# Optimization experiments

Measured on AMD Instinct MI355X. Metric: run time of the kernel, lower is better.

Reference implementation:

```python
import jax, jax.numpy as jnp
import numpy as np

B, N, K, H, NC, NL = 512, 128, 16, 16, 6, 4  # batch, atoms, neighbors/atom, h_a, classes, EGNN layers

def _lin(key, fi, fo):
    lim = 1.0 / np.sqrt(fi)
    return jax.random.uniform(key, (fi, fo), jnp.float32, -lim, lim)

def _bias(key, fi, fo):
    lim = 1.0 / np.sqrt(fi)
    return jax.random.uniform(key, (fo,), jnp.float32, -lim, lim)

def setup_inputs():
    key = jax.random.key(0)
    kc, ke, ki, ko, kf, kl = jax.random.split(key, 6)
    coords = jax.random.normal(kc, (B, N, 3), dtype=jnp.float32)
    # fixed adjacency: node i -> (i+1 .. i+K) mod N, same for every frame
    adj = np.zeros((N, N), dtype=np.float32)
    idx = np.arange(N)
    for d in range(1, K + 1):
        adj[idx, (idx + d) % N] = 1.0
    data = jnp.concatenate([coords, jnp.broadcast_to(jnp.asarray(adj), (B, N, N))], axis=-1)  # [B,N,3+N]
    # edge-index construction (host-side; matches torch (edge_inds>0).nonzero().t(), row/col += offset*N)
    off, r, c = np.nonzero(np.broadcast_to(adj > 0.0, (B, N, N)))
    row = jnp.asarray(r + off * N, dtype=jnp.int32)
    col = jnp.asarray(c + off * N, dtype=jnp.int32)
    emb_w = jax.random.normal(ke, (N, H), dtype=jnp.float32)  # atom_emb.weight.data.normal_()
    k1, k2 = jax.random.split(ki); ein_w, ein_b = _lin(k1, H, H), _bias(k2, H, H)
    k1, k2 = jax.random.split(ko); eout_w, eout_b = _lin(k1, H, H), _bias(k2, H, H)
    k1, k2 = jax.random.split(kf); fc_w, fc_b = _lin(k1, H, NC), _bias(k2, H, NC)
    def make_layer(k):
        ks = jax.random.split(k, 11)
        xav = 0.001 * np.sqrt(6.0 / (H + 1))  # coord_mlp last layer: xavier_uniform gain=0.001, no bias
        return dict(
            e1_w=_lin(ks[0], 2 * H + 2, H), e1_b=_bias(ks[1], 2 * H + 2, H),
            e2_w=_lin(ks[2], H, H),        e2_b=_bias(ks[3], H, H),
            n1_w=_lin(ks[4], 2 * H, H),    n1_b=_bias(ks[5], 2 * H, H),
            n2_w=_lin(ks[6], H, H),        n2_b=_bias(ks[7], H, H),
            c1_w=_lin(ks[8], H, H),        c1_b=_bias(ks[9], H, H),
            c2_w=jax.random.uniform(ks[10], (H, 1), jnp.float32, -xav, xav))
    layers = [make_layer(k) for k in jax.random.split(kl, NL)]
    stacked = {name: jnp.stack([l[name] for l in layers]) for name in layers[0]}  # [NL, ...]
    out = dict(data=data, row=row, col=col, emb_w=emb_w, ein_w=ein_w, ein_b=ein_b,
               eout_w=eout_w, eout_b=eout_b, fc_w=fc_w, fc_b=fc_b)
    out.update(stacked)
    return out

def reference(data, row, col, emb_w, ein_w, ein_b, eout_w, eout_b, fc_w, fc_b,
              e1_w, e1_b, e2_w, e2_b, n1_w, n1_b, n2_w, n2_b, c1_w, c1_b, c2_w):
    Bn = data.shape[0] * data.shape[1]  # B*N flattened nodes
    silu = jax.nn.silu
    seg = lambda v: jax.ops.segment_sum(v, row, num_segments=Bn)
    # atom_emb(arange(N)) repeated over batch -> tile embedding table rows
    h = jnp.broadcast_to(emb_w[None, :, :], (data.shape[0], data.shape[1], H)).reshape(Bn, H)
    x = data[:, :, :3].reshape(Bn, 3).astype(jnp.float32)
    e_attr = jnp.ones((row.shape[0], 1), jnp.float32)
    cnt = jnp.maximum(seg(jnp.ones((row.shape[0],), jnp.float32)), 1.0)[:, None]  # for coords_agg='mean'
    h = h @ ein_w + ein_b  # embedding_in
    for l in range(NL):  # E_GCL layers (residual=True, attention=False)
        cd = x[row] - x[col]                                  # [E,3] coord_diff
        radial = jnp.sum(cd * cd, axis=1, keepdims=True)      # [E,1]
        ein = jnp.concatenate([h[row], h[col], radial, e_attr], axis=1)  # [E, 2H+2]
        m = silu(silu(ein @ e1_w[l] + e1_b[l]) @ e2_w[l] + e2_b[l])      # edge_mlp -> [E,H]
        t = silu(m @ c1_w[l] + c1_b[l]) @ c2_w[l]             # coord_mlp -> [E,1]
        x = x + seg(cd * t) / cnt                             # mean-aggregated coord update
        agg_m = seg(m)                                        # scatter-add messages to nodes
        h = h + (silu(jnp.concatenate([h, agg_m], axis=1) @ n1_w[l] + n1_b[l]) @ n2_w[l] + n2_b[l])
    h = h @ eout_w + eout_b  # embedding_out
    prot = jnp.sum(h.reshape(data.shape[0], data.shape[1], H), axis=1) / N  # pooling
    return jax.nn.softmax(prot @ fc_w + fc_b, axis=-1)
```

## Files before the change

kernel.cpp:

```cpp
#include <hip/hip_runtime.h>
#include <math.h>


#define NB   512
#define NT   512
#define NN   128
#define HH   16
#define NCLS 6
#define NLAY 4
#define PAD  20

#define W_E1   0
#define W_E1B  544
#define W_E2   560
#define W_E2B  816
#define W_C1   832
#define W_C1B  1088
#define W_C2   1104
#define W_N1   1120
#define W_N1B  1632
#define W_N2   1648
#define W_N2B  1904
#define W_TOT  1920

__device__ __forceinline__ float silu_f(float v) {
    return __fdividef(v, 1.f + __expf(-v));
}

extern "C" __global__ __launch_bounds__(512, 4)
void GraphVampNet_73624329388105_kernel(
    const float* __restrict__ data,
    const float* __restrict__ emb_w,
    const float* __restrict__ ein_w, const float* __restrict__ ein_b,
    const float* __restrict__ eout_w, const float* __restrict__ eout_b,
    const float* __restrict__ fc_w,  const float* __restrict__ fc_b,
    const float* __restrict__ e1_w,  const float* __restrict__ e1_b,
    const float* __restrict__ e2_w,  const float* __restrict__ e2_b,
    const float* __restrict__ n1_w,  const float* __restrict__ n1_b,
    const float* __restrict__ n2_w,  const float* __restrict__ n2_b,
    const float* __restrict__ c1_w,  const float* __restrict__ c1_b,
    const float* __restrict__ c2_w,
    float* __restrict__ out)
{
    __shared__ float h[NN][PAD];
    __shared__ float xs[NN][4];
    __shared__ float pB[NN][PAD];
    __shared__ __align__(16) float un[384 * PAD];
    __shared__ __align__(16) float wb[W_TOT];
    __shared__ float hp[HH];
    __shared__ float prot[HH];

    const int b = blockIdx.x;
    const int t = threadIdx.x;

    if (t < NN) {
        const float* dp = data + ((size_t)b * NN + t) * (NN + 3);
        xs[t][0] = dp[0]; xs[t][1] = dp[1]; xs[t][2] = dp[2]; xs[t][3] = 0.f;

        float ev[HH];
        #pragma unroll
        for (int k = 0; k < HH; k++) ev[k] = emb_w[t * HH + k];
        float acc[HH];
        #pragma unroll
        for (int o = 0; o < HH; o++) acc[o] = ein_b[o];
        #pragma unroll
        for (int k = 0; k < HH; k++) {
            const float v = ev[k];
            #pragma unroll
            for (int o = 0; o < HH; o++) acc[o] += v * ein_w[k * HH + o];
        }
        #pragma unroll
        for (int o = 0; o < HH; o++) h[t][o] = acc[o];
    }

    const int i = t & (NN - 1);
    const int q = t >> 7;

    for (int l = 0; l < NLAY; l++) {
        {
            const float* E1W = e1_w + l * 34 * HH;
            wb[W_E1 + t] = E1W[t];
            if (t < 32) wb[W_E1 + 512 + t] = E1W[512 + t];
            wb[W_N1 + t] = n1_w[l * 2 * HH * HH + t];
            if (t < 256) {
                wb[W_E2 + t] = e2_w[l * HH * HH + t];
                wb[W_C1 + t] = c1_w[l * HH * HH + t];
                wb[W_N2 + t] = n2_w[l * HH * HH + t];
            }
            if (t < HH) {
                wb[W_E1B + t] = e1_b[l * HH + t];
                wb[W_E2B + t] = e2_b[l * HH + t];
                wb[W_C1B + t] = c1_b[l * HH + t];
                wb[W_C2  + t] = c2_w[l * HH + t];
                wb[W_N1B + t] = n1_b[l * HH + t];
                wb[W_N2B + t] = n2_b[l * HH + t];
            }
        }
        __syncthreads();

        if (t < 2 * NN) {
            const int node = t & (NN - 1);
            float hv[HH];
            #pragma unroll
            for (int k = 0; k < HH; k++) hv[k] = h[node][k];
            if (t < NN) {
                float acc[HH];
                #pragma unroll
                for (int o = 0; o < HH; o++) acc[o] = wb[W_E1B + o] + wb[W_E1 + 33 * HH + o];
                #pragma unroll
                for (int k = 0; k < HH; k++) {
                    const float v = hv[k];
                    #pragma unroll
                    for (int o = 0; o < HH; o++) acc[o] += v * wb[W_E1 + k * HH + o];
                }
                #pragma unroll
                for (int o = 0; o < HH; o++) un[node * PAD + o] = acc[o];
            } else {
                float acc[HH];
                #pragma unroll
                for (int o = 0; o < HH; o++) acc[o] = 0.f;
                #pragma unroll
                for (int k = 0; k < HH; k++) {
                    const float v = hv[k];
                    #pragma unroll
                    for (int o = 0; o < HH; o++) acc[o] += v * wb[W_E1 + (16 + k) * HH + o];
                }
                #pragma unroll
                for (int o = 0; o < HH; o++) pB[node][o] = acc[o];
            }
        }
        __syncthreads();

        float aggm[HH];
        #pragma unroll
        for (int o = 0; o < HH; o++) aggm[o] = 0.f;
        float cx0 = 0.f, cx1 = 0.f, cx2 = 0.f;
        {
            const float4 xi = *(const float4*)&xs[i][0];

            #pragma unroll 1
            for (int g = 0; g < 2; g++) {
                unsigned o_col = W_E1 + 32 * HH;
                unsigned o_e2  = W_E2,  o_e2b = W_E2B;
                unsigned o_c1  = W_C1,  o_c1b = W_C1B;
                unsigned o_c2  = W_C2;
                unsigned o_pa  = (unsigned)(i * PAD);
                asm volatile("" : "+v"(o_col), "+v"(o_e2), "+v"(o_e2b),
                                  "+v"(o_c1), "+v"(o_c1b), "+v"(o_c2), "+v"(o_pa));

                const int dbase = q * 4 + g * 2 + 1;
                const int j0 = (i + dbase) & (NN - 1);
                const int j1 = (i + dbase + 1) & (NN - 1);
                const float4 xj0 = *(const float4*)&xs[j0][0];
                const float4 xj1 = *(const float4*)&xs[j1][0];
                const float a00 = xi.x - xj0.x, a01 = xi.y - xj0.y, a02 = xi.z - xj0.z;
                const float a10 = xi.x - xj1.x, a11 = xi.y - xj1.y, a12 = xi.z - xj1.z;
                const float r0 = a00 * a00 + a01 * a01 + a02 * a02;
                const float r1 = a10 * a10 + a11 * a11 + a12 * a12;

                float m0[HH], m1v[HH];
                #pragma unroll
                for (int qq = 0; qq < 4; qq++) {
                    const float4 pa = ((const float4*)(un + o_pa))[qq];
                    const float4 wc = ((const float4*)(wb + o_col))[qq];
                    const float4 p0 = *(const float4*)&pB[j0][qq * 4];
                    const float4 p1 = *(const float4*)&pB[j1][qq * 4];
                    m0[qq*4+0]  = silu_f(pa.x + p0.x + r0 * wc.x);
                    m0[qq*4+1]  = silu_f(pa.y + p0.y + r0 * wc.y);
                    m0[qq*4+2]  = silu_f(pa.z + p0.z + r0 * wc.z);
                    m0[qq*4+3]  = silu_f(pa.w + p0.w + r0 * wc.w);
                    m1v[qq*4+0] = silu_f(pa.x + p1.x + r1 * wc.x);
                    m1v[qq*4+1] = silu_f(pa.y + p1.y + r1 * wc.y);
                    m1v[qq*4+2] = silu_f(pa.z + p1.z + r1 * wc.z);
                    m1v[qq*4+3] = silu_f(pa.w + p1.w + r1 * wc.w);
                }

                float ac0[HH], ac1[HH];
                #pragma unroll
                for (int qq = 0; qq < 4; qq++) {
                    const float4 bb = ((const float4*)(wb + o_e2b))[qq];
                    ac0[qq*4+0] = bb.x; ac0[qq*4+1] = bb.y; ac0[qq*4+2] = bb.z; ac0[qq*4+3] = bb.w;
                    ac1[qq*4+0] = bb.x; ac1[qq*4+1] = bb.y; ac1[qq*4+2] = bb.z; ac1[qq*4+3] = bb.w;
                }
                #pragma unroll
                for (int k = 0; k < HH; k++) {
                    const float v0 = m0[k], v1 = m1v[k];
                    #pragma unroll
                    for (int qq = 0; qq < 4; qq++) {
                        const float4 w = ((const float4*)(wb + o_e2))[k * 4 + qq];
                        ac0[qq*4+0] += v0 * w.x; ac0[qq*4+1] += v0 * w.y;
                        ac0[qq*4+2] += v0 * w.z; ac0[qq*4+3] += v0 * w.w;
                        ac1[qq*4+0] += v1 * w.x; ac1[qq*4+1] += v1 * w.y;
                        ac1[qq*4+2] += v1 * w.z; ac1[qq*4+3] += v1 * w.w;
                    }
                }
                #pragma unroll
                for (int o = 0; o < HH; o++) {
                    m0[o]  = silu_f(ac0[o]);
                    m1v[o] = silu_f(ac1[o]);
                    aggm[o] += m0[o] + m1v[o];
                }

                #pragma unroll
                for (int qq = 0; qq < 4; qq++) {
                    const float4 bb = ((const float4*)(wb + o_c1b))[qq];
                    ac0[qq*4+0] = bb.x; ac0[qq*4+1] = bb.y; ac0[qq*4+2] = bb.z; ac0[qq*4+3] = bb.w;
                    ac1[qq*4+0] = bb.x; ac1[qq*4+1] = bb.y; ac1[qq*4+2] = bb.z; ac1[qq*4+3] = bb.w;
                }
                #pragma unroll
                for (int k = 0; k < HH; k++) {
                    const float v0 = m0[k], v1 = m1v[k];
                    #pragma unroll
                    for (int qq = 0; qq < 4; qq++) {
                        const float4 w = ((const float4*)(wb + o_c1))[k * 4 + qq];
                        ac0[qq*4+0] += v0 * w.x; ac0[qq*4+1] += v0 * w.y;
                        ac0[qq*4+2] += v0 * w.z; ac0[qq*4+3] += v0 * w.w;
                        ac1[qq*4+0] += v1 * w.x; ac1[qq*4+1] += v1 * w.y;
                        ac1[qq*4+2] += v1 * w.z; ac1[qq*4+3] += v1 * w.w;
                    }
                }
                float t0 = 0.f, t1 = 0.f;
                #pragma unroll
                for (int qq = 0; qq < 4; qq++) {
                    const float4 cw = ((const float4*)(wb + o_c2))[qq];
                    t0 += silu_f(ac0[qq*4+0]) * cw.x + silu_f(ac0[qq*4+1]) * cw.y
                        + silu_f(ac0[qq*4+2]) * cw.z + silu_f(ac0[qq*4+3]) * cw.w;
                    t1 += silu_f(ac1[qq*4+0]) * cw.x + silu_f(ac1[qq*4+1]) * cw.y
                        + silu_f(ac1[qq*4+2]) * cw.z + silu_f(ac1[qq*4+3]) * cw.w;
                }

                cx0 += a00 * t0 + a10 * t1;
                cx1 += a01 * t0 + a11 * t1;
                cx2 += a02 * t0 + a12 * t1;
            }
        }
        __syncthreads();

        if (t >= NN) {
            const int r = t - NN;
            #pragma unroll
            for (int o = 0; o < HH; o++) un[r * PAD + o] = aggm[o];
            float4 cxv; cxv.x = cx0; cxv.y = cx1; cxv.z = cx2; cxv.w = 0.f;
            *(float4*)(un + r * PAD + 16) = cxv;
        }
        __syncthreads();

        if (t < NN) {
            float aggt[HH];
            #pragma unroll
            for (int o = 0; o < HH; o++)
                aggt[o] = aggm[o] + un[t * PAD + o] + un[(t + 128) * PAD + o]
                        + un[(t + 256) * PAD + o];
            const float sx0 = cx0 + un[t * PAD + 16] + un[(t + 128) * PAD + 16]
                            + un[(t + 256) * PAD + 16];
            const float sx1 = cx1 + un[t * PAD + 17] + un[(t + 128) * PAD + 17]
                            + un[(t + 256) * PAD + 17];
            const float sx2 = cx2 + un[t * PAD + 18] + un[(t + 128) * PAD + 18]
                            + un[(t + 256) * PAD + 18];

            float hv[HH];
            #pragma unroll
            for (int k = 0; k < HH; k++) hv[k] = h[t][k];

            float acc[HH];
            #pragma unroll
            for (int o = 0; o < HH; o++) acc[o] = wb[W_N1B + o];
            #pragma unroll
            for (int k = 0; k < HH; k++) {
                const float v = hv[k];
                #pragma unroll
                for (int o = 0; o < HH; o++) acc[o] += v * wb[W_N1 + k * HH + o];
            }
            #pragma unroll
            for (int k = 0; k < HH; k++) {
                const float v = aggt[k];
                #pragma unroll
                for (int o = 0; o < HH; o++) acc[o] += v * wb[W_N1 + (16 + k) * HH + o];
            }
            float u[HH];
            #pragma unroll
            for (int o = 0; o < HH; o++) u[o] = silu_f(acc[o]);

            float acc2[HH];
            #pragma unroll
            for (int o = 0; o < HH; o++) acc2[o] = wb[W_N2B + o];
            #pragma unroll
            for (int k = 0; k < HH; k++) {
                const float v = u[k];
                #pragma unroll
                for (int o = 0; o < HH; o++) acc2[o] += v * wb[W_N2 + k * HH + o];
            }
            #pragma unroll
            for (int o = 0; o < HH; o++) h[t][o] = hv[o] + acc2[o];

            const float inv = 1.f / 16.f;
            xs[t][0] += sx0 * inv;
            xs[t][1] += sx1 * inv;
            xs[t][2] += sx2 * inv;
        }
        __syncthreads();
    }

    if (t < HH) {
        float acc = 0.f;
        for (int n = 0; n < NN; n++) acc += h[n][t];
        hp[t] = acc * (1.f / NN);
    }
    __syncthreads();
    if (t < HH) {
        float acc = eout_b[t];
        #pragma unroll
        for (int k = 0; k < HH; k++) acc += hp[k] * eout_w[k * HH + t];
        prot[t] = acc;
    }
    __syncthreads();
    if (t == 0) {
        float lg[NCLS];
        float mx = -1e30f;
        #pragma unroll
        for (int c = 0; c < NCLS; c++) {
            float acc = fc_b[c];
            #pragma unroll
            for (int k = 0; k < HH; k++) acc += prot[k] * fc_w[k * NCLS + c];
            lg[c] = acc;
            mx = fmaxf(mx, acc);
        }
        float s = 0.f;
        #pragma unroll
        for (int c = 0; c < NCLS; c++) { lg[c] = __expf(lg[c] - mx); s += lg[c]; }
        const float invs = 1.f / s;
        #pragma unroll
        for (int c = 0; c < NCLS; c++) out[b * NCLS + c] = lg[c] * invs;
    }
}

extern "C" void kernel_launch(void* const* d_in, const int* in_sizes, int n_in,
                              void* d_out, int out_size, void* d_ws, size_t ws_size,
                              hipStream_t stream) {
    const float* data   = (const float*)d_in[0];
    const float* emb_w  = (const float*)d_in[3];
    const float* ein_w  = (const float*)d_in[4];
    const float* ein_b  = (const float*)d_in[5];
    const float* eout_w = (const float*)d_in[6];
    const float* eout_b = (const float*)d_in[7];
    const float* fc_w   = (const float*)d_in[8];
    const float* fc_b   = (const float*)d_in[9];
    const float* e1_w   = (const float*)d_in[10];
    const float* e1_b   = (const float*)d_in[11];
    const float* e2_w   = (const float*)d_in[12];
    const float* e2_b   = (const float*)d_in[13];
    const float* n1_w   = (const float*)d_in[14];
    const float* n1_b   = (const float*)d_in[15];
    const float* n2_w   = (const float*)d_in[16];
    const float* n2_b   = (const float*)d_in[17];
    const float* c1_w   = (const float*)d_in[18];
    const float* c1_b   = (const float*)d_in[19];
    const float* c2_w   = (const float*)d_in[20];

    GraphVampNet_73624329388105_kernel<<<NB, NT, 0, stream>>>(
        data, emb_w, ein_w, ein_b, eout_w, eout_b, fc_w, fc_b,
        e1_w, e1_b, e2_w, e2_b, n1_w, n1_b, n2_w, n2_b, c1_w, c1_b, c2_w,
        (float*)d_out);
}
```

Baseline: 385.3 us.

## Use 384 threads per block with uneven 6/5/5 edge split per node

Cuts the block from 512 to 384 threads, so each node's 16 neighbor edges are split across three thread groups (6, 5 and 5 edges) instead of four groups of 4. Each thread now runs three two-edge iterations, and odd leftover edges are masked with a multiplier, so some redundant edge MLP work is computed and discarded. The per-node pA row is also hoisted into registers once before the loop, and the reduction buffer shrinks to two partial rows. The goal is to reduce the shared-memory partial-reduction work and change occupancy, at the cost of wasted compute on masked edges, fewer threads per block and a lower launch-bounds occupancy hint.

Measured after the change: 424.6 us. +10.2%, slower.

```diff
diff --git a/kernel.cpp b/kernel.cpp
--- a/kernel.cpp
+++ b/kernel.cpp
@@ -3,7 +3,7 @@
 
 
 #define NB   512
-#define NT   512
+#define NT   384
 #define NN   128
 #define HH   16
 #define NCLS 6
@@ -27,7 +27,7 @@
     return __fdividef(v, 1.f + __expf(-v));
 }
 
-extern "C" __global__ __launch_bounds__(512, 4)
+extern "C" __global__ __launch_bounds__(384, 2)
 void GraphVampNet_73624329388105_kernel(
     const float* __restrict__ data,
     const float* __restrict__ emb_w,
@@ -45,13 +45,15 @@
     __shared__ float h[NN][PAD];
     __shared__ float xs[NN][4];
     __shared__ float pB[NN][PAD];
-    __shared__ __align__(16) float un[384 * PAD];
+    __shared__ __align__(16) float un[256 * PAD];
     __shared__ __align__(16) float wb[W_TOT];
     __shared__ float hp[HH];
     __shared__ float prot[HH];
 
     const int b = blockIdx.x;
     const int t = threadIdx.x;
+    const int i = t & (NN - 1);
+    const int q = t >> 7;
 
     if (t < NN) {
         const float* dp = data + ((size_t)b * NN + t) * (NN + 3);
@@ -73,15 +75,17 @@
         for (int o = 0; o < HH; o++) h[t][o] = acc[o];
     }
 
-    const int i = t & (NN - 1);
-    const int q = t >> 7;
+    const int dstart = (q == 0) ? 1 : ((q == 1) ? 7 : 12);
+    const int dend   = (q == 0) ? 6 : ((q == 1) ? 11 : 16);
 
     for (int l = 0; l < NLAY; l++) {
         {
             const float* E1W = e1_w + l * 34 * HH;
             wb[W_E1 + t] = E1W[t];
-            if (t < 32) wb[W_E1 + 512 + t] = E1W[512 + t];
-            wb[W_N1 + t] = n1_w[l * 2 * HH * HH + t];
+            if (t < 160) wb[W_E1 + 384 + t] = E1W[384 + t];
+            const float* N1W = n1_w + l * 2 * HH * HH;
+            wb[W_N1 + t] = N1W[t];
+            if (t < 128) wb[W_N1 + 384 + t] = N1W[384 + t];
             if (t < 256) {
                 wb[W_E2 + t] = e2_w[l * HH * HH + t];
                 wb[W_C1 + t] = c1_w[l * HH * HH + t];
@@ -136,21 +140,25 @@
         for (int o = 0; o < HH; o++) aggm[o] = 0.f;
         float cx0 = 0.f, cx1 = 0.f, cx2 = 0.f;
         {
+            float pAi[HH];
+            #pragma unroll
+            for (int o = 0; o < HH; o++) pAi[o] = un[i * PAD + o];
             const float4 xi = *(const float4*)&xs[i][0];
 
             #pragma unroll 1
-            for (int g = 0; g < 2; g++) {
+            for (int g = 0; g < 3; g++) {
                 unsigned o_col = W_E1 + 32 * HH;
                 unsigned o_e2  = W_E2,  o_e2b = W_E2B;
                 unsigned o_c1  = W_C1,  o_c1b = W_C1B;
                 unsigned o_c2  = W_C2;
-                unsigned o_pa  = (unsigned)(i * PAD);
                 asm volatile("" : "+v"(o_col), "+v"(o_e2), "+v"(o_e2b),
-                                  "+v"(o_c1), "+v"(o_c1b), "+v"(o_c2), "+v"(o_pa));
-
-                const int dbase = q * 4 + g * 2 + 1;
-                const int j0 = (i + dbase) & (NN - 1);
-                const int j1 = (i + dbase + 1) & (NN - 1);
+                                  "+v"(o_c1), "+v"(o_c1b), "+v"(o_c2));
+
+                const int d0 = dstart + 2 * g;
+                const int d1 = d0 + 1;
+                const float s1 = (d1 <= dend) ? 1.f : 0.f;
+                const int j0 = (i + d0) & (NN - 1);
+                const int j1 = (i + d1) & (NN - 1);
                 const float4 xj0 = *(const float4*)&xs[j0][0];
                 const float4 xj1 = *(const float4*)&xs[j1][0];
                 const float a00 = xi.x - xj0.x, a01 = xi.y - xj0.y, a02 = xi.z - xj0.z;
@@ -161,18 +169,17 @@
                 float m0[HH], m1v[HH];
                 #pragma unroll
                 for (int qq = 0; qq < 4; qq++) {
-                    const float4 pa = ((const float4*)(un + o_pa))[qq];
                     const float4 wc = ((const float4*)(wb + o_col))[qq];
                     const float4 p0 = *(const float4*)&pB[j0][qq * 4];
                     const float4 p1 = *(const float4*)&pB[j1][qq * 4];
-                    m0[qq*4+0]  = silu_f(pa.x + p0.x + r0 * wc.x);
-                    m0[qq*4+1]  = silu_f(pa.y + p0.y + r0 * wc.y);
-                    m0[qq*4+2]  = silu_f(pa.z + p0.z + r0 * wc.z);
-                    m0[qq*4+3]  = silu_f(pa.w + p0.w + r0 * wc.w);
-                    m1v[qq*4+0] = silu_f(pa.x + p1.x + r1 * wc.x);
-                    m1v[qq*4+1] = silu_f(pa.y + p1.y + r1 * wc.y);
-                    m1v[qq*4+2] = silu_f(pa.z + p1.z + r1 * wc.z);
-                    m1v[qq*4+3] = silu_f(pa.w + p1.w + r1 * wc.w);
+                    m0[qq*4+0]  = silu_f(pAi[qq*4+0] + p0.x + r0 * wc.x);
+                    m0[qq*4+1]  = silu_f(pAi[qq*4+1] + p0.y + r0 * wc.y);
+                    m0[qq*4+2]  = silu_f(pAi[qq*4+2] + p0.z + r0 * wc.z);
+                    m0[qq*4+3]  = silu_f(pAi[qq*4+3] + p0.w + r0 * wc.w);
+                    m1v[qq*4+0] = silu_f(pAi[qq*4+0] + p1.x + r1 * wc.x);
+                    m1v[qq*4+1] = silu_f(pAi[qq*4+1] + p1.y + r1 * wc.y);
+                    m1v[qq*4+2] = silu_f(pAi[qq*4+2] + p1.z + r1 * wc.z);
+                    m1v[qq*4+3] = silu_f(pAi[qq*4+3] + p1.w + r1 * wc.w);
                 }
 
                 float ac0[HH], ac1[HH];
@@ -198,7 +205,7 @@
                 for (int o = 0; o < HH; o++) {
                     m0[o]  = silu_f(ac0[o]);
                     m1v[o] = silu_f(ac1[o]);
-                    aggm[o] += m0[o] + m1v[o];
+                    aggm[o] += m0[o] + s1 * m1v[o];
                 }
 
                 #pragma unroll
@@ -229,9 +236,9 @@
                         + silu_f(ac1[qq*4+2]) * cw.z + silu_f(ac1[qq*4+3]) * cw.w;
                 }
 
-                cx0 += a00 * t0 + a10 * t1;
-                cx1 += a01 * t0 + a11 * t1;
-                cx2 += a02 * t0 + a12 * t1;
+                cx0 += a00 * t0 + s1 * (a10 * t1);
+                cx1 += a01 * t0 + s1 * (a11 * t1);
+                cx2 += a02 * t0 + s1 * (a12 * t1);
             }
         }
         __syncthreads();
@@ -249,14 +256,10 @@
             float aggt[HH];
             #pragma unroll
             for (int o = 0; o < HH; o++)
-                aggt[o] = aggm[o] + un[t * PAD + o] + un[(t + 128) * PAD + o]
-                        + un[(t + 256) * PAD + o];
-            const float sx0 = cx0 + un[t * PAD + 16] + un[(t + 128) * PAD + 16]
-                            + un[(t + 256) * PAD + 16];
-            const float sx1 = cx1 + un[t * PAD + 17] + un[(t + 128) * PAD + 17]
-                            + un[(t + 256) * PAD + 17];
-            const float sx2 = cx2 + un[t * PAD + 18] + un[(t + 128) * PAD + 18]
-                            + un[(t + 256) * PAD + 18];
+                aggt[o] = aggm[o] + un[t * PAD + o] + un[(t + 128) * PAD + o];
+            const float sx0 = cx0 + un[t * PAD + 16] + un[(t + 128) * PAD + 16];
+            const float sx1 = cx1 + un[t * PAD + 17] + un[(t + 128) * PAD + 17];
+            const float sx2 = cx2 + un[t * PAD + 18] + un[(t + 128) * PAD + 18];
 
             float hv[HH];
             #pragma unroll
```
